# Optimization experiments

Measured on AMD Instinct MI355X. Metric: run time of the kernel, lower is better.

## Reference

```python
import jax, jax.numpy as jnp
import numpy as np

B, C, H, W = 8, 256, 48, 48
RED = 1  # reduction
CR = C // RED
CG = C // 4  # fuse gate hidden channels


def conv1x1(x, w):
    # x: [B,C,H,W], w: [O,C] -> [B,O,H,W]
    return jnp.einsum('oc,bchw->bohw', w, x)


def conv3x3(x, w, b):
    # x: [B,Ci,H,W], w: [O,Ci,3,3], b: [O]
    y = jax.lax.conv_general_dilated(
        x, w, window_strides=(1, 1), padding='SAME',
        dimension_numbers=('NCHW', 'OIHW', 'NCHW'))
    return y + b[None, :, None, None]


def cross_attention(source, guidance, wq, wk, wv, bv, gamma):
    b, c, h, w = source.shape
    hw = h * w
    Q = conv1x1(source, wq).reshape(b, -1, hw)      # [B,CR,HW]
    K = conv1x1(guidance, wk).reshape(b, -1, hw)    # [B,CR,HW]
    V = (conv1x1(guidance, wv) + bv[None, :, None, None]).reshape(b, c, hw)
    energy = jnp.einsum('bqn,bqm->bnm', Q, K)       # [B,HW,HW]
    attn = jax.nn.softmax(energy, axis=-1)
    out = jnp.einsum('bcm,bnm->bcn', V, attn)       # [B,C,HW]
    return gamma * out.reshape(b, c, h, w) + source


def setup_inputs() -> dict:
    key = jax.random.key(0)
    ks = jax.random.split(key, 16)
    s = lambda fan_in: 1.0 / np.sqrt(fan_in)
    d = {
        'x1': jax.random.normal(ks[0], (B, C, H, W), jnp.float32),
        'x2': jax.random.normal(ks[1], (B, C, H, W), jnp.float32),
        'wq1': jax.random.normal(ks[2], (CR, C), jnp.float32) * s(C),
        'wk1': jax.random.normal(ks[3], (CR, C), jnp.float32) * s(C),
        'wv1': jax.random.normal(ks[4], (C, C), jnp.float32) * s(C),
        'bv1': jax.random.normal(ks[5], (C,), jnp.float32) * s(C),
        'gamma1': jax.random.normal(ks[6], (1,), jnp.float32) * 0.1,
        'wq2': jax.random.normal(ks[7], (CR, C), jnp.float32) * s(C),
        'wk2': jax.random.normal(ks[8], (CR, C), jnp.float32) * s(C),
        'wv2': jax.random.normal(ks[9], (C, C), jnp.float32) * s(C),
        'bv2': jax.random.normal(ks[10], (C,), jnp.float32) * s(C),
        'gamma2': jax.random.normal(ks[11], (1,), jnp.float32) * 0.1,
        'fw1': jax.random.normal(ks[12], (CG, 2 * C, 3, 3), jnp.float32) * s(2 * C * 9),
        'fb1': jnp.zeros((CG,), jnp.float32),
        'fw2': jax.random.normal(ks[13], (2, CG, 3, 3), jnp.float32) * s(CG * 9),
        'fb2': jnp.zeros((2,), jnp.float32),
    }
    return d


def reference(x1, x2, wq1, wk1, wv1, bv1, gamma1, wq2, wk2, wv2, bv2, gamma2,
              fw1, fb1, fw2, fb2):
    att_x1 = cross_attention(x1, x2, wq1, wk1, wv1, bv1, gamma1)
    att_x2 = cross_attention(x2, x1, wq2, wk2, wv2, bv2, gamma2)
    cat = jnp.concatenate([att_x1, att_x2], axis=1)  # [B,2C,H,W]
    h = jax.nn.relu(conv3x3(cat, fw1, fb1))
    gates = jax.nn.softmax(conv3x3(h, fw2, fb2), axis=1)  # [B,2,H,W]
    return gates[:, 0:1] * att_x1 + gates[:, 1:2] * att_x2
```

## Files before the change

### kernel.cpp

```cpp
#include <hip/hip_runtime.h>

namespace {

constexpr int BATCH = 8;
constexpr int CH    = 256;
constexpr int HW    = 2304;
constexpr int IMG   = 48;
constexpr int CG    = 64;

typedef __bf16 bf16x8 __attribute__((ext_vector_type(8)));
typedef __bf16 bf16x4 __attribute__((ext_vector_type(4)));
typedef float  f32x4  __attribute__((ext_vector_type(4)));

constexpr int ROWB = 40;
constexpr int KSTRD = 136;
constexpr int PSTRD = 136;
constexpr int CSTR = 40;

constexpr size_t BF_SLAB = (size_t)BATCH * HW * CH * 2;
constexpr size_t QT1_OFF = 0;
constexpr size_t KT1_OFF = 1 * BF_SLAB;
constexpr size_t VB1_OFF = 2 * BF_SLAB;
constexpr size_t QT2_OFF = 3 * BF_SLAB;
constexpr size_t KT2_OFF = 4 * BF_SLAB;
constexpr size_t VB2_OFF = 5 * BF_SLAB;
constexpr size_t AT_OFF  = 6 * BF_SLAB;
constexpr size_t A1_OFF  = AT_OFF + (size_t)BATCH * HW * 512 * 2;
constexpr size_t A2_OFF  = A1_OFF + (size_t)BATCH * CH * HW * 4;
constexpr size_t HB_OFF  = A2_OFF + (size_t)BATCH * CH * HW * 4;
constexpr size_t G0_OFF  = HB_OFF + (size_t)BATCH * CG * HW * 4;
constexpr size_t WT_OFF  = G0_OFF + (size_t)BATCH * HW * 4;

__device__ __forceinline__ void stage_f32(const float* __restrict__ src, size_t srcStride,
                                          __bf16* dst, int t) {
    const int r = t & 127, s = t >> 7;
    const float4* sp = reinterpret_cast<const float4*>(src + (size_t)r * srcStride + s * 16);
    float4 f0 = sp[0], f1 = sp[1], f2 = sp[2], f3 = sp[3];
    bf16x8 v0, v1;
    v0[0]=(__bf16)f0.x; v0[1]=(__bf16)f0.y; v0[2]=(__bf16)f0.z; v0[3]=(__bf16)f0.w;
    v0[4]=(__bf16)f1.x; v0[5]=(__bf16)f1.y; v0[6]=(__bf16)f1.z; v0[7]=(__bf16)f1.w;
    v1[0]=(__bf16)f2.x; v1[1]=(__bf16)f2.y; v1[2]=(__bf16)f2.z; v1[3]=(__bf16)f2.w;
    v1[4]=(__bf16)f3.x; v1[5]=(__bf16)f3.y; v1[6]=(__bf16)f3.z; v1[7]=(__bf16)f3.w;
    bf16x8* dp = reinterpret_cast<bf16x8*>(dst + r * ROWB + s * 16);
    dp[0] = v0;
    dp[1] = v1;
}

__device__ __forceinline__ void frag_step(const __bf16* As, const __bf16* Bs,
                                          f32x4 (&acc)[4][4], int lane, int wm, int wn) {
    const int r = lane & 15, g = lane >> 4;
    bf16x8 a[4], b[4];
#pragma unroll
    for (int i = 0; i < 4; ++i) {
        a[i] = *reinterpret_cast<const bf16x8*>(As + (wm * 64 + i * 16 + r) * ROWB + g * 8);
        b[i] = *reinterpret_cast<const bf16x8*>(Bs + (wn * 64 + i * 16 + r) * ROWB + g * 8);
    }
#pragma unroll
    for (int i = 0; i < 4; ++i)
#pragma unroll
        for (int j = 0; j < 4; ++j)
            acc[i][j] = __builtin_amdgcn_mfma_f32_16x16x32_bf16(a[i], b[j], acc[i][j], 0, 0, 0);
}

__global__ __launch_bounds__(256) void proj3_mfma(
    const float* __restrict__ Xsrc, const float* __restrict__ Xg,
    const float* __restrict__ wq, const float* __restrict__ wk,
    const float* __restrict__ wv, const float* __restrict__ bv,
    __bf16* __restrict__ QT, __bf16* __restrict__ KT, __bf16* __restrict__ VB)
{
    __shared__ __bf16 As[128 * ROWB];
    __shared__ __bf16 Bs[128 * ROWB];
    const int p = blockIdx.z >> 3;
    const int b = blockIdx.z & 7;
    const float* W = (p == 0) ? wq : (p == 1) ? wk : wv;
    const float* X = (p == 0) ? Xsrc : Xg;
    const float* Xb = X + (size_t)b * CH * HW;

    const int t = threadIdx.x;
    const int lane = t & 63, wid = t >> 6;
    const int wm = wid >> 1, wn = wid & 1;
    const int m0 = blockIdx.y * 128, n0 = blockIdx.x * 128;

    f32x4 acc[4][4] = {};
    const int nB = t & 127, halfB = t >> 7;

    for (int k0 = 0; k0 < CH; k0 += 32) {
        stage_f32(W + (size_t)m0 * CH + k0, CH, As, t);
        float v[16];
#pragma unroll
        for (int kk = 0; kk < 16; ++kk)
            v[kk] = Xb[(size_t)(k0 + halfB * 16 + kk) * HW + n0 + nB];
        bf16x8 p0, p1;
#pragma unroll
        for (int kk = 0; kk < 8; ++kk) { p0[kk] = (__bf16)v[kk]; p1[kk] = (__bf16)v[kk + 8]; }
        bf16x8* dp = reinterpret_cast<bf16x8*>(Bs + nB * ROWB + halfB * 16);
        dp[0] = p0; dp[1] = p1;
        __syncthreads();
        frag_step(As, Bs, acc, lane, wm, wn);
        __syncthreads();
    }

    const int g = lane >> 4, r = lane & 15;
    if (p < 2) {
        __bf16* T = (p == 0) ? QT : KT;
#pragma unroll
        for (int mi = 0; mi < 4; ++mi)
#pragma unroll
            for (int nj = 0; nj < 4; ++nj) {
                const int mb = m0 + wm * 64 + mi * 16 + g * 4;
                const int n  = n0 + wn * 64 + nj * 16 + r;
                bf16x4 pk;
#pragma unroll
                for (int q = 0; q < 4; ++q) pk[q] = (__bf16)acc[mi][nj][q];
                *reinterpret_cast<bf16x4*>(T + ((size_t)b * HW + n) * CH + mb) = pk;
            }
    } else {
#pragma unroll
        for (int mi = 0; mi < 4; ++mi)
#pragma unroll
            for (int nj = 0; nj < 4; ++nj) {
                const int mb = m0 + wm * 64 + mi * 16 + g * 4;
                const int n  = n0 + wn * 64 + nj * 16 + r;
#pragma unroll
                for (int q = 0; q < 4; ++q)
                    VB[((size_t)b * CH + mb + q) * HW + n] = (__bf16)(acc[mi][nj][q] + bv[mb + q]);
            }
    }
}

__global__ __launch_bounds__(256, 2) void fused_flash(
    const __bf16* __restrict__ QT1, const __bf16* __restrict__ KT1, const __bf16* __restrict__ VB1,
    const __bf16* __restrict__ QT2, const __bf16* __restrict__ KT2, const __bf16* __restrict__ VB2,
    const float* __restrict__ x1, const float* __restrict__ x2,
    const float* __restrict__ g1, const float* __restrict__ g2,
    float* __restrict__ A1, float* __restrict__ A2, __bf16* __restrict__ AT)
{
    __shared__ __bf16 Ks[128 * KSTRD];
    __shared__ __bf16 P_lds[64 * PSTRD];
    __shared__ float  sc_lds[64];

    const int bid  = blockIdx.x;
    const int work = (bid & 7) * 72 + (bid >> 3);
    const int z = work / 36, ntile = work - z * 36;

    const int att = z >> 3, b = z & 7;
    const __bf16* QT = att ? QT2 : QT1;
    const __bf16* KT = att ? KT2 : KT1;
    const __bf16* VB = att ? VB2 : VB1;
    const float* src = att ? x2 : x1;
    const float* gmp = att ? g2 : g1;
    float* A         = att ? A2 : A1;
    const int aoff   = att ? CH : 0;

    const int t = threadIdx.x, lane = t & 63, w = t >> 6;
    const int r = lane & 15, g = lane >> 4;
    const int n0 = ntile * 64;
    const __bf16* KTb = KT + (size_t)b * HW * CH;
    const __bf16* VBb = VB + (size_t)b * CH * HW;

    bf16x8 qf[8];
    {
        const __bf16* qrow = QT + ((size_t)b * HW + n0 + w * 16 + r) * CH;
#pragma unroll
        for (int kc = 0; kc < 8; ++kc)
            qf[kc] = *reinterpret_cast<const bf16x8*>(qrow + kc * 32 + g * 8);
    }

    const int kr = t >> 1, kcol = (t & 1) * 64;
    bf16x8 kbuf[8];
    {
        const bf16x8* sp = reinterpret_cast<const bf16x8*>(KTb + (size_t)kr * CH + kcol);
#pragma unroll
        for (int u = 0; u < 8; ++u) kbuf[u] = sp[u];
    }

    float m_run = -3.0e38f;
    float s_run = 0.f;
    f32x4 accO[4][4] = {};

    for (int m0 = 0; m0 < HW; m0 += 128) {
        f32x4 accS[8] = {};
        {
            bf16x8* dp = reinterpret_cast<bf16x8*>(Ks + kr * KSTRD + kcol);
#pragma unroll
            for (int u = 0; u < 8; ++u) dp[u] = kbuf[u];
        }
        __syncthreads();
        {
            const bf16x8* sp = reinterpret_cast<const bf16x8*>(
                KTb + (size_t)(m0 + kr) * CH + 128 + kcol);
#pragma unroll
            for (int u = 0; u < 8; ++u) kbuf[u] = sp[u];
        }
        __builtin_amdgcn_s_setprio(1);
#pragma unroll
        for (int kk = 0; kk < 4; ++kk) {
            const bf16x8 qv = qf[kk];
#pragma unroll
            for (int j = 0; j < 8; ++j) {
                const bf16x8 kf = *reinterpret_cast<const bf16x8*>(
                    Ks + (j * 16 + r) * KSTRD + kk * 32 + g * 8);
                accS[j] = __builtin_amdgcn_mfma_f32_16x16x32_bf16(kf, qv, accS[j], 0, 0, 0);
            }
        }
        __builtin_amdgcn_s_setprio(0);
        __syncthreads();
        {
            bf16x8* dp = reinterpret_cast<bf16x8*>(Ks + kr * KSTRD + kcol);
#pragma unroll
            for (int u = 0; u < 8; ++u) dp[u] = kbuf[u];
        }
        __syncthreads();
        {
            const int m0n = (m0 + 128 < HW) ? (m0 + 128) : 0;
            const bf16x8* sp = reinterpret_cast<const bf16x8*>(
                KTb + (size_t)(m0n + kr) * CH + kcol);
#pragma unroll
            for (int u = 0; u < 8; ++u) kbuf[u] = sp[u];
        }
        bf16x8 av0[8];
#pragma unroll
        for (int kk = 0; kk < 2; ++kk)
#pragma unroll
            for (int i = 0; i < 4; ++i)
                av0[kk * 4 + i] = *reinterpret_cast<const bf16x8*>(
                    VBb + (size_t)(w * 64 + i * 16 + r) * HW + m0 + kk * 32 + g * 8);
        __builtin_amdgcn_s_setprio(1);
#pragma unroll
        for (int kk = 0; kk < 4; ++kk) {
            const bf16x8 qv = qf[4 + kk];
#pragma unroll
            for (int j = 0; j < 8; ++j) {
                const bf16x8 kf = *reinterpret_cast<const bf16x8*>(
                    Ks + (j * 16 + r) * KSTRD + kk * 32 + g * 8);
                accS[j] = __builtin_amdgcn_mfma_f32_16x16x32_bf16(kf, qv, accS[j], 0, 0, 0);
            }
        }
        __builtin_amdgcn_s_setprio(0);
        {
            float mj[8];
#pragma unroll
            for (int j = 0; j < 8; ++j)
                mj[j] = fmaxf(fmaxf(accS[j][0], accS[j][1]), fmaxf(accS[j][2], accS[j][3]));
            float m03 = fmaxf(fmaxf(mj[0], mj[1]), fmaxf(mj[2], mj[3]));
            float m47 = fmaxf(fmaxf(mj[4], mj[5]), fmaxf(mj[6], mj[7]));
            float tmax = fmaxf(m03, m47);
            tmax = fmaxf(tmax, __shfl_xor(tmax, 16));
            tmax = fmaxf(tmax, __shfl_xor(tmax, 32));
            const float nm = fmaxf(m_run, tmax);
            float tsj[8];
#pragma unroll
            for (int j = 0; j < 8; ++j) {
                const float pe0 = __expf(accS[j][0] - nm);
                const float pe1 = __expf(accS[j][1] - nm);
                const float pe2 = __expf(accS[j][2] - nm);
                const float pe3 = __expf(accS[j][3] - nm);
                tsj[j] = (pe0 + pe1) + (pe2 + pe3);
                bf16x4 pk;
                pk[0] = (__bf16)pe0; pk[1] = (__bf16)pe1;
                pk[2] = (__bf16)pe2; pk[3] = (__bf16)pe3;
                *reinterpret_cast<bf16x4*>(
                    P_lds + (w * 16 + r) * PSTRD + j * 16 + g * 4) = pk;
            }
            float ts = ((tsj[0] + tsj[1]) + (tsj[2] + tsj[3])) +
                       ((tsj[4] + tsj[5]) + (tsj[6] + tsj[7]));
            ts += __shfl_xor(ts, 16);
            ts += __shfl_xor(ts, 32);
            const float scale = __expf(m_run - nm);
            s_run = s_run * scale + ts;
            m_run = nm;
            if (lane < 16) sc_lds[w * 16 + r] = scale;
        }
        __syncthreads();
        {
            float scj[4];
#pragma unroll
            for (int j = 0; j < 4; ++j) scj[j] = sc_lds[j * 16 + r];
#pragma unroll
            for (int i = 0; i < 4; ++i)
#pragma unroll
                for (int j = 0; j < 4; ++j)
#pragma unroll
                    for (int q = 0; q < 4; ++q) accO[i][j][q] *= scj[j];
        }
        bf16x8 av1[8];
#pragma unroll
        for (int kk = 0; kk < 2; ++kk)
#pragma unroll
            for (int i = 0; i < 4; ++i)
                av1[kk * 4 + i] = *reinterpret_cast<const bf16x8*>(
                    VBb + (size_t)(w * 64 + i * 16 + r) * HW + m0 + 64 + kk * 32 + g * 8);
        __builtin_amdgcn_s_setprio(1);
#pragma unroll
        for (int kk = 0; kk < 2; ++kk) {
            bf16x8 bp[4];
#pragma unroll
            for (int j = 0; j < 4; ++j)
                bp[j] = *reinterpret_cast<const bf16x8*>(
                    P_lds + (j * 16 + r) * PSTRD + kk * 32 + g * 8);
#pragma unroll
            for (int i = 0; i < 4; ++i)
#pragma unroll
                for (int j = 0; j < 4; ++j)
                    accO[i][j] = __builtin_amdgcn_mfma_f32_16x16x32_bf16(
                        av0[kk * 4 + i], bp[j], accO[i][j], 0, 0, 0);
        }
#pragma unroll
        for (int kk = 0; kk < 2; ++kk) {
            bf16x8 bp[4];
#pragma unroll
            for (int j = 0; j < 4; ++j)
                bp[j] = *reinterpret_cast<const bf16x8*>(
                    P_lds + (j * 16 + r) * PSTRD + 64 + kk * 32 + g * 8);
#pragma unroll
            for (int i = 0; i < 4; ++i)
#pragma unroll
                for (int j = 0; j < 4; ++j)
                    accO[i][j] = __builtin_amdgcn_mfma_f32_16x16x32_bf16(
                        av1[kk * 4 + i], bp[j], accO[i][j], 0, 0, 0);
        }
        __builtin_amdgcn_s_setprio(0);
    }

    if (lane < 16) sc_lds[w * 16 + r] = 1.f / s_run;
    __syncthreads();
    float IS_l[4];
#pragma unroll
    for (int j = 0; j < 4; ++j) IS_l[j] = sc_lds[j * 16 + r];
    const float gm = gmp[0];
#pragma unroll
    for (int i = 0; i < 4; ++i)
#pragma unroll
        for (int j = 0; j < 4; ++j) {
            const int cb = w * 64 + i * 16 + g * 4;
            const int n  = n0 + j * 16 + r;
            const float sc = gm * IS_l[j];
            float vals[4];
#pragma unroll
            for (int q = 0; q < 4; ++q) {
                const size_t idx = ((size_t)b * CH + cb + q) * HW + n;
                vals[q] = sc * accO[i][j][q] + src[idx];
                A[idx] = vals[q];
            }
            bf16x4 pk;
#pragma unroll
            for (int q = 0; q < 4; ++q) pk[q] = (__bf16)vals[q];
            *reinterpret_cast<bf16x4*>(AT + ((size_t)b * HW + n) * 512 + aoff + cb) = pk;
        }
}

__global__ __launch_bounds__(256) void wprep(const float* __restrict__ fw1,
                                             __bf16* __restrict__ WT)
{
    const int i = blockIdx.x * 256 + threadIdx.x;
    const int tap = i >> 15;
    const int rem = i & 32767;
    const int m = rem >> 9, c = rem & 511;
    WT[i] = (__bf16)fw1[(size_t)m * 4608 + c * 9 + tap];
}

__global__ __launch_bounds__(256) void conv1_v2(
    const __bf16* __restrict__ AT, const __bf16* __restrict__ WT,
    float* __restrict__ P4)
{
    __shared__ __bf16 A9[9 * 64 * CSTR];
    __shared__ __bf16 HALO[240 * CSTR];
    const int kc = blockIdx.y, b = blockIdx.z, n0 = blockIdx.x * 128;
    const int t = threadIdx.x, lane = t & 63, wid = t >> 6;
    const int r = lane & 15, g = lane >> 4;

    int yj[2], xj[2];
#pragma unroll
    for (int j = 0; j < 2; ++j) {
        const int p = n0 + wid * 32 + j * 16 + r;
        yj[j] = p / IMG; xj[j] = p - yj[j] * IMG;
    }

    f32x4 acc[4][2] = {};

#pragma unroll 1
    for (int st = 0; st < 4; ++st) {
        const int cbase = kc * 128 + st * 32;
        if (t < 240) {
            const int nn = n0 - 56 + t;
            bf16x8 h0 = {}, h1 = {}, h2 = {}, h3 = {};
            if (nn >= 0 && nn < HW) {
                const bf16x8* sp = reinterpret_cast<const bf16x8*>(
                    AT + ((size_t)b * HW + nn) * 512 + cbase);
                h0 = sp[0]; h1 = sp[1]; h2 = sp[2]; h3 = sp[3];
            }
            bf16x8* dp = reinterpret_cast<bf16x8*>(HALO + t * CSTR);
            dp[0] = h0; dp[1] = h1; dp[2] = h2; dp[3] = h3;
        }
        {
            const int m = t >> 2, seg = t & 3;
#pragma unroll
            for (int tap = 0; tap < 9; ++tap)
                *reinterpret_cast<bf16x8*>(A9 + (tap * 64 + m) * CSTR + seg * 8) =
                    *reinterpret_cast<const bf16x8*>(WT + ((size_t)tap * 64 + m) * 512 + cbase + seg * 8);
        }
        __syncthreads();
#pragma unroll 1
        for (int tap = 0; tap < 9; ++tap) {
            const int dy = tap / 3 - 1;
            const int dx = tap - (tap / 3) * 3 - 1;
            bf16x8 bb[2];
#pragma unroll
            for (int j = 0; j < 2; ++j) {
                const bool valid = ((unsigned)(yj[j] + dy) < (unsigned)IMG) &&
                                   ((unsigned)(xj[j] + dx) < (unsigned)IMG);
                const int row = wid * 32 + j * 16 + r + 56 + dy * IMG + dx;
                bf16x8 v = {};
                if (valid) v = *reinterpret_cast<const bf16x8*>(HALO + row * CSTR + g * 8);
                bb[j] = v;
            }
            bf16x8 a[4];
#pragma unroll
            for (int i = 0; i < 4; ++i)
                a[i] = *reinterpret_cast<const bf16x8*>(A9 + (tap * 64 + i * 16 + r) * CSTR + g * 8);
#pragma unroll
            for (int i = 0; i < 4; ++i)
#pragma unroll
                for (int j = 0; j < 2; ++j)
                    acc[i][j] = __builtin_amdgcn_mfma_f32_16x16x32_bf16(a[i], bb[j], acc[i][j], 0, 0, 0);
        }
        __syncthreads();
    }
#pragma unroll
    for (int mi = 0; mi < 4; ++mi)
#pragma unroll
        for (int nj = 0; nj < 2; ++nj) {
            const int m = mi * 16 + g * 4;
            const int n = n0 + wid * 32 + nj * 16 + r;
#pragma unroll
            for (int q = 0; q < 4; ++q)
                P4[(((size_t)kc * BATCH + b) * CG + m + q) * HW + n] = acc[mi][nj][q];
        }
}

__global__ __launch_bounds__(256) void reduce_hb(
    const float* __restrict__ P4, const float* __restrict__ fb1,
    float* __restrict__ HB)
{
    const int idx = blockIdx.x * 256 + threadIdx.x;
    constexpr size_t STRIDE = (size_t)BATCH * CG * HW;
    const int m = (idx / HW) & 63;
    float s = P4[idx] + P4[idx + STRIDE] + P4[idx + 2 * STRIDE] + P4[idx + 3 * STRIDE];
    HB[idx] = fmaxf(s + fb1[m], 0.f);
}

__global__ __launch_bounds__(256) void gates_v2(
    const float* __restrict__ hbuf, const float* __restrict__ fw2,
    const float* __restrict__ fb2, float* __restrict__ g0buf)
{
    __shared__ float w2s[1152];
    __shared__ float par[2][4][64];
    const int t = threadIdx.x;
    for (int i = t; i < 1152; i += 256) w2s[i] = fw2[i];
    __syncthreads();
    const int px = t & 63, grp = t >> 6;
    const int idx = blockIdx.x * 64 + px;
    const int b = idx / HW;
    const int n = idx - b * HW;
    const int y = n / IMG, x = n - (n / IMG) * IMG;
    float c0 = 0.f, c1 = 0.f;
    const float* hb = hbuf + ((size_t)b * CG + grp * 16) * HW;
    for (int ci = 0; ci < 16; ++ci) {
        const float* hp = hb + (size_t)ci * HW;
        const float* w0 = &w2s[(grp * 16 + ci) * 9];
        const float* w1 = &w2s[576 + (grp * 16 + ci) * 9];
#pragma unroll
        for (int tap = 0; tap < 9; ++tap) {
            const int dy = tap / 3 - 1, dx = tap % 3 - 1;
            const int yy = y + dy, xx = x + dx;
            if (yy >= 0 && yy < IMG && xx >= 0 && xx < IMG) {
                const float hv = hp[yy * IMG + xx];
                c0 = fmaf(hv, w0[tap], c0);
                c1 = fmaf(hv, w1[tap], c1);
            }
        }
    }
    par[0][grp][px] = c0;
    par[1][grp][px] = c1;
    __syncthreads();
    if (t < 64) {
        const float s0 = par[0][0][t] + par[0][1][t] + par[0][2][t] + par[0][3][t] + fb2[0];
        const float s1 = par[1][0][t] + par[1][1][t] + par[1][2][t] + par[1][3][t] + fb2[1];
        g0buf[blockIdx.x * 64 + t] = 1.f / (1.f + __expf(s1 - s0));
    }
}

__global__ __launch_bounds__(256) void blend_kernel(
    const float* __restrict__ att1, const float* __restrict__ att2,
    const float* __restrict__ g0buf, float* __restrict__ out)
{
    const int i = blockIdx.x * 256 + threadIdx.x;
    const int r = i / 576;
    const int q = i - r * 576;
    const int b = r >> 8;
    const float4 a1 = reinterpret_cast<const float4*>(att1)[i];
    const float4 a2 = reinterpret_cast<const float4*>(att2)[i];
    const float4 g  = *reinterpret_cast<const float4*>(&g0buf[(size_t)b * HW + q * 4]);
    float4 o;
    o.x = g.x * a1.x + (1.f - g.x) * a2.x;
    o.y = g.y * a1.y + (1.f - g.y) * a2.y;
    o.z = g.z * a1.z + (1.f - g.z) * a2.z;
    o.w = g.w * a1.w + (1.f - g.w) * a2.w;
    reinterpret_cast<float4*>(out)[i] = o;
}

}

extern "C" void kernel_launch(void* const* d_in, const int* in_sizes, int n_in,
                              void* d_out, int out_size, void* d_ws, size_t ws_size,
                              hipStream_t stream)
{
    const float* x1  = (const float*)d_in[0];
    const float* x2  = (const float*)d_in[1];
    const float* wq1 = (const float*)d_in[2];
    const float* wk1 = (const float*)d_in[3];
    const float* wv1 = (const float*)d_in[4];
    const float* bv1 = (const float*)d_in[5];
    const float* g1  = (const float*)d_in[6];
    const float* wq2 = (const float*)d_in[7];
    const float* wk2 = (const float*)d_in[8];
    const float* wv2 = (const float*)d_in[9];
    const float* bv2 = (const float*)d_in[10];
    const float* g2  = (const float*)d_in[11];
    const float* fw1 = (const float*)d_in[12];
    const float* fb1 = (const float*)d_in[13];
    const float* fw2 = (const float*)d_in[14];
    const float* fb2 = (const float*)d_in[15];
    float* out = (float*)d_out;
    char*  wsb = (char*)d_ws;

    __bf16* QT1 = (__bf16*)(wsb + QT1_OFF);
    __bf16* KT1 = (__bf16*)(wsb + KT1_OFF);
    __bf16* VB1 = (__bf16*)(wsb + VB1_OFF);
    __bf16* QT2 = (__bf16*)(wsb + QT2_OFF);
    __bf16* KT2 = (__bf16*)(wsb + KT2_OFF);
    __bf16* VB2 = (__bf16*)(wsb + VB2_OFF);
    __bf16* AT  = (__bf16*)(wsb + AT_OFF);
    float*  A1  = (float*)(wsb + A1_OFF);
    float*  A2  = (float*)(wsb + A2_OFF);
    float*  HB  = (float*)(wsb + HB_OFF);
    float*  G0  = (float*)(wsb + G0_OFF);
    __bf16* WT  = (__bf16*)(wsb + WT_OFF);
    float*  P4  = (float*)(wsb + QT1_OFF);

    (void)in_sizes; (void)n_in; (void)out_size; (void)ws_size;

    proj3_mfma<<<dim3(18, 2, 24), 256, 0, stream>>>(x1, x2, wq1, wk1, wv1, bv1, QT1, KT1, VB1);
    proj3_mfma<<<dim3(18, 2, 24), 256, 0, stream>>>(x2, x1, wq2, wk2, wv2, bv2, QT2, KT2, VB2);
    wprep<<<dim3(1152), 256, 0, stream>>>(fw1, WT);

    fused_flash<<<dim3(576), 256, 0, stream>>>(
        QT1, KT1, VB1, QT2, KT2, VB2, x1, x2, g1, g2, A1, A2, AT);

    conv1_v2<<<dim3(18, 4, 8), 256, 0, stream>>>(AT, WT, P4);
    reduce_hb<<<dim3(4608), 256, 0, stream>>>(P4, fb1, HB);
    gates_v2<<<dim3(288), 256, 0, stream>>>(HB, fw2, fb2, G0);
    blend_kernel<<<dim3(4608), 256, 0, stream>>>(A1, A2, G0, out);
}
```

Baseline: 396.3 us.

## Store V in 32-column blocked layout and hoist both V fragment loads

The V projection output is now written in a blocked layout where each group of 32 spatial positions forms a contiguous [256 ch x 32] tile. The flash attention kernel's V fragment reads then hit contiguous 64-byte rows instead of rows strided by HW. The second half of the V loads (av1) is also moved up next to the first, so both are issued before the QK MFMAs and their latency is hidden. The cost is higher register pressure in a kernel launched with 2 waves per SIMD, plus a more scattered store pattern in the projection epilogue.

```diff
diff --git a/kernel.cpp b/kernel.cpp
--- a/kernel.cpp
+++ b/kernel.cpp
@@ -20,10 +20,10 @@
 constexpr size_t BF_SLAB = (size_t)BATCH * HW * CH * 2;
 constexpr size_t QT1_OFF = 0;
 constexpr size_t KT1_OFF = 1 * BF_SLAB;
-constexpr size_t VB1_OFF = 2 * BF_SLAB;
+constexpr size_t VF1_OFF = 2 * BF_SLAB;
 constexpr size_t QT2_OFF = 3 * BF_SLAB;
 constexpr size_t KT2_OFF = 4 * BF_SLAB;
-constexpr size_t VB2_OFF = 5 * BF_SLAB;
+constexpr size_t VF2_OFF = 5 * BF_SLAB;
 constexpr size_t AT_OFF  = 6 * BF_SLAB;
 constexpr size_t A1_OFF  = AT_OFF + (size_t)BATCH * HW * 512 * 2;
 constexpr size_t A2_OFF  = A1_OFF + (size_t)BATCH * CH * HW * 4;
@@ -66,7 +66,7 @@
     const float* __restrict__ Xsrc, const float* __restrict__ Xg,
     const float* __restrict__ wq, const float* __restrict__ wk,
     const float* __restrict__ wv, const float* __restrict__ bv,
-    __bf16* __restrict__ QT, __bf16* __restrict__ KT, __bf16* __restrict__ VB)
+    __bf16* __restrict__ QT, __bf16* __restrict__ KT, __bf16* __restrict__ VF)
 {
     __shared__ __bf16 As[128 * ROWB];
     __shared__ __bf16 Bs[128 * ROWB];
@@ -115,22 +115,25 @@
                 *reinterpret_cast<bf16x4*>(T + ((size_t)b * HW + n) * CH + mb) = pk;
             }
     } else {
+        __bf16* VFb = VF + (size_t)b * CH * HW;
 #pragma unroll
         for (int mi = 0; mi < 4; ++mi)
 #pragma unroll
             for (int nj = 0; nj < 4; ++nj) {
                 const int mb = m0 + wm * 64 + mi * 16 + g * 4;
                 const int n  = n0 + wn * 64 + nj * 16 + r;
+                const size_t base = ((size_t)(n >> 5) * 256);
 #pragma unroll
                 for (int q = 0; q < 4; ++q)
-                    VB[((size_t)b * CH + mb + q) * HW + n] = (__bf16)(acc[mi][nj][q] + bv[mb + q]);
+                    VFb[(base + mb + q) * 32 + (n & 31)] =
+                        (__bf16)(acc[mi][nj][q] + bv[mb + q]);
             }
     }
 }
 
 __global__ __launch_bounds__(256, 2) void fused_flash(
-    const __bf16* __restrict__ QT1, const __bf16* __restrict__ KT1, const __bf16* __restrict__ VB1,
-    const __bf16* __restrict__ QT2, const __bf16* __restrict__ KT2, const __bf16* __restrict__ VB2,
+    const __bf16* __restrict__ QT1, const __bf16* __restrict__ KT1, const __bf16* __restrict__ VF1,
+    const __bf16* __restrict__ QT2, const __bf16* __restrict__ KT2, const __bf16* __restrict__ VF2,
     const float* __restrict__ x1, const float* __restrict__ x2,
     const float* __restrict__ g1, const float* __restrict__ g2,
     float* __restrict__ A1, float* __restrict__ A2, __bf16* __restrict__ AT)
@@ -146,7 +149,7 @@
     const int att = z >> 3, b = z & 7;
     const __bf16* QT = att ? QT2 : QT1;
     const __bf16* KT = att ? KT2 : KT1;
-    const __bf16* VB = att ? VB2 : VB1;
+    const __bf16* VF = att ? VF2 : VF1;
     const float* src = att ? x2 : x1;
     const float* gmp = att ? g2 : g1;
     float* A         = att ? A2 : A1;
@@ -156,7 +159,7 @@
     const int r = lane & 15, g = lane >> 4;
     const int n0 = ntile * 64;
     const __bf16* KTb = KT + (size_t)b * HW * CH;
-    const __bf16* VBb = VB + (size_t)b * CH * HW;
+    const __bf16* VFb = VF + (size_t)b * CH * HW;
 
     bf16x8 qf[8];
     {
@@ -218,13 +221,19 @@
 #pragma unroll
             for (int u = 0; u < 8; ++u) kbuf[u] = sp[u];
         }
-        bf16x8 av0[8];
-#pragma unroll
-        for (int kk = 0; kk < 2; ++kk)
-#pragma unroll
-            for (int i = 0; i < 4; ++i)
-                av0[kk * 4 + i] = *reinterpret_cast<const bf16x8*>(
-                    VBb + (size_t)(w * 64 + i * 16 + r) * HW + m0 + kk * 32 + g * 8);
+        bf16x8 av0[8], av1[8];
+        {
+            const size_t mcb = (size_t)(m0 >> 5) * 256;
+#pragma unroll
+            for (int kk = 0; kk < 2; ++kk)
+#pragma unroll
+                for (int i = 0; i < 4; ++i) {
+                    av0[kk * 4 + i] = *reinterpret_cast<const bf16x8*>(
+                        VFb + ((mcb + (size_t)kk * 256) + w * 64 + i * 16 + r) * 32 + g * 8);
+                    av1[kk * 4 + i] = *reinterpret_cast<const bf16x8*>(
+                        VFb + ((mcb + (size_t)(kk + 2) * 256) + w * 64 + i * 16 + r) * 32 + g * 8);
+                }
+        }
         __builtin_amdgcn_s_setprio(1);
 #pragma unroll
         for (int kk = 0; kk < 4; ++kk) {
@@ -283,13 +292,6 @@
 #pragma unroll
                     for (int q = 0; q < 4; ++q) accO[i][j][q] *= scj[j];
         }
-        bf16x8 av1[8];
-#pragma unroll
-        for (int kk = 0; kk < 2; ++kk)
-#pragma unroll
-            for (int i = 0; i < 4; ++i)
-                av1[kk * 4 + i] = *reinterpret_cast<const bf16x8*>(
-                    VBb + (size_t)(w * 64 + i * 16 + r) * HW + m0 + 64 + kk * 32 + g * 8);
         __builtin_amdgcn_s_setprio(1);
 #pragma unroll
         for (int kk = 0; kk < 2; ++kk) {
@@ -536,10 +538,10 @@
 
     __bf16* QT1 = (__bf16*)(wsb + QT1_OFF);
     __bf16* KT1 = (__bf16*)(wsb + KT1_OFF);
-    __bf16* VB1 = (__bf16*)(wsb + VB1_OFF);
+    __bf16* VF1 = (__bf16*)(wsb + VF1_OFF);
     __bf16* QT2 = (__bf16*)(wsb + QT2_OFF);
     __bf16* KT2 = (__bf16*)(wsb + KT2_OFF);
-    __bf16* VB2 = (__bf16*)(wsb + VB2_OFF);
+    __bf16* VF2 = (__bf16*)(wsb + VF2_OFF);
     __bf16* AT  = (__bf16*)(wsb + AT_OFF);
     float*  A1  = (float*)(wsb + A1_OFF);
     float*  A2  = (float*)(wsb + A2_OFF);
@@ -550,12 +552,12 @@
 
     (void)in_sizes; (void)n_in; (void)out_size; (void)ws_size;
 
-    proj3_mfma<<<dim3(18, 2, 24), 256, 0, stream>>>(x1, x2, wq1, wk1, wv1, bv1, QT1, KT1, VB1);
-    proj3_mfma<<<dim3(18, 2, 24), 256, 0, stream>>>(x2, x1, wq2, wk2, wv2, bv2, QT2, KT2, VB2);
+    proj3_mfma<<<dim3(18, 2, 24), 256, 0, stream>>>(x1, x2, wq1, wk1, wv1, bv1, QT1, KT1, VF1);
+    proj3_mfma<<<dim3(18, 2, 24), 256, 0, stream>>>(x2, x1, wq2, wk2, wv2, bv2, QT2, KT2, VF2);
     wprep<<<dim3(1152), 256, 0, stream>>>(fw1, WT);
 
     fused_flash<<<dim3(576), 256, 0, stream>>>(
-        QT1, KT1, VB1, QT2, KT2, VB2, x1, x2, g1, g2, A1, A2, AT);
+        QT1, KT1, VF1, QT2, KT2, VF2, x1, x2, g1, g2, A1, A2, AT);
 
     conv1_v2<<<dim3(18, 4, 8), 256, 0, stream>>>(AT, WT, P4);
     reduce_hb<<<dim3(4608), 256, 0, stream>>>(P4, fb1, HB);
```

Result: slower. 406.6 us (+2.6%).
